# Optimization experiments

Hardware: AMD Instinct MI355X
Metric: run time of the kernel (lower is better)

## Reference

```python
import jax, jax.numpy as jnp
import numpy as np

D_MODEL, D_BLOOM, N_HEADS = 768, 64, 4
HEAD_DIM = D_MODEL // N_HEADS


def setup_inputs() -> dict:
    key = jax.random.key(0)
    ks = jax.random.split(key, 16)
    B, S = 8, 1024
    s = 0.02
    return {
        "dnabert_hidden": jax.random.normal(ks[0], (B, S, D_MODEL), jnp.float32),
        "bloom_encoding": jax.random.uniform(ks[1], (B, S, D_BLOOM), jnp.float32),
        "Wq": jax.random.normal(ks[2], (D_MODEL, D_MODEL), jnp.float32) * s,
        "bq": jnp.zeros((D_MODEL,), jnp.float32),
        "Wk": jax.random.normal(ks[3], (D_BLOOM, D_MODEL), jnp.float32) * s,
        "bk": jnp.zeros((D_MODEL,), jnp.float32),
        "Wv": jax.random.normal(ks[4], (D_MODEL, D_MODEL), jnp.float32) * s,
        "bv": jnp.zeros((D_MODEL,), jnp.float32),
        "Wb1": jax.random.normal(ks[5], (D_BLOOM, N_HEADS * 2), jnp.float32) * s,
        "bb1": jnp.zeros((N_HEADS * 2,), jnp.float32),
        "Wb2": jax.random.normal(ks[6], (N_HEADS * 2, N_HEADS), jnp.float32) * s,
        "bb2": jnp.zeros((N_HEADS,), jnp.float32),
        "Wo": jax.random.normal(ks[7], (D_MODEL, D_MODEL), jnp.float32) * s,
        "bo": jnp.zeros((D_MODEL,), jnp.float32),
        "ln_g": jnp.ones((D_MODEL,), jnp.float32),
        "ln_b": jnp.zeros((D_MODEL,), jnp.float32),
    }


def reference(dnabert_hidden, bloom_encoding, Wq, bq, Wk, bk, Wv, bv,
              Wb1, bb1, Wb2, bb2, Wo, bo, ln_g, ln_b):
    B, S, _ = dnabert_hidden.shape
    H, Dh = N_HEADS, HEAD_DIM
    # projections -> [B, H, S, Dh]
    Q = (dnabert_hidden @ Wq + bq).reshape(B, S, H, Dh).transpose(0, 2, 1, 3)
    K = (bloom_encoding @ Wk + bk).reshape(B, S, H, Dh).transpose(0, 2, 1, 3)
    V = (dnabert_hidden @ Wv + bv).reshape(B, S, H, Dh).transpose(0, 2, 1, 3)
    scores = jnp.einsum('bhqd,bhkd->bhqk', Q, K) / jnp.sqrt(jnp.float32(Dh))
    # bloom bias MLP: [B, S, H] -> broadcast over query positions as [B, H, 1, S]
    h = jax.nn.gelu(bloom_encoding @ Wb1 + bb1, approximate=False)
    bias = (h @ Wb2 + bb2).transpose(0, 2, 1)[:, :, None, :]
    attn = jax.nn.softmax(scores + bias, axis=-1)  # dropout is identity in eval
    ctx = jnp.einsum('bhqk,bhkd->bhqd', attn, V)
    ctx = ctx.transpose(0, 2, 1, 3).reshape(B, S, H * Dh)
    out = ctx @ Wo + bo
    x = out + dnabert_hidden
    mu = jnp.mean(x, axis=-1, keepdims=True)
    var = jnp.var(x, axis=-1, keepdims=True)
    y = (x - mu) * jax.lax.rsqrt(var + 1e-5) * ln_g + ln_b
    return y, attn
```

## Files before the change

### kernel.cpp

```cpp
#include <hip/hip_runtime.h>
#include <hip/hip_bf16.h>
#include <math.h>
#include <stdint.h>

typedef __bf16 bf16;
typedef __bf16 bf16x8 __attribute__((ext_vector_type(8)));
typedef __bf16 bf16x4v __attribute__((ext_vector_type(4)));
typedef float f32x4 __attribute__((ext_vector_type(4)));

#define NHEADS 4
#define DM 768
#define DB 64
#define HD 192
#define BATCH 8
#define SEQ 1024
#define MROWS 8192
#define SCALE 0.07216878364870323f

__device__ __forceinline__ void gld_lds16(const void* g, void* l) {
  __builtin_amdgcn_global_load_lds(
      (__attribute__((address_space(1))) void*)(void*)g,
      (__attribute__((address_space(3))) void*)l, 16, 0, 0);
}

__global__ __launch_bounds__(256) void prologue(
    const float* __restrict__ Xd, bf16* __restrict__ Xd_bf,
    const float* __restrict__ Xb, bf16* __restrict__ Xb_bf,
    const float* __restrict__ Wq, const float* __restrict__ Wv,
    const float* __restrict__ Wk, const float* __restrict__ Wo,
    bf16* __restrict__ WT0, bf16* __restrict__ WT1,
    bf16* __restrict__ WT2, bf16* __restrict__ WT3,
    const float* __restrict__ Wb1, const float* __restrict__ bb1,
    const float* __restrict__ Wb2, const float* __restrict__ bb2,
    float* __restrict__ biasarr) {
  const int id = blockIdx.x;
  const int tid = threadIdx.x;
  if (id < 6656) {
    const float* in = (id < 6144) ? Xd : Xb;
    bf16* out = (id < 6144) ? Xd_bf : Xb_bf;
    long i = (long)(id < 6144 ? id : id - 6144) * 256 + tid;
    f32x4 v = *(const f32x4*)&in[i * 4];
    bf16x4v t;
    t[0] = (bf16)v[0]; t[1] = (bf16)v[1]; t[2] = (bf16)v[2]; t[3] = (bf16)v[3];
    *(bf16x4v*)&out[i * 4] = t;
  } else if (id < 6688) {
    int idx = (id - 6656) * 256 + tid;
    const float* x = Xb + (long)idx * DB;
    float h[8];
#pragma unroll
    for (int j = 0; j < 8; ++j) h[j] = bb1[j];
    for (int k = 0; k < DB; ++k) {
      float xv = x[k];
#pragma unroll
      for (int j = 0; j < 8; ++j) h[j] = fmaf(xv, Wb1[k * 8 + j], h[j]);
    }
#pragma unroll
    for (int j = 0; j < 8; ++j) {
      float a = h[j];
      h[j] = 0.5f * a * (1.0f + erff(a * 0.7071067811865476f));
    }
    int b = idx >> 10, s = idx & 1023;
#pragma unroll
    for (int o = 0; o < 4; ++o) {
      float a = bb2[o];
#pragma unroll
      for (int j = 0; j < 8; ++j) a = fmaf(h[j], Wb2[j * 4 + o], a);
      biasarr[((long)(b * 4 + o) << 10) + s] = a;
    }
  } else {
    int wi = id - 6688;
    const float* W;
    bf16* WT;
    int K, base;
    if (wi < 2304)      { W = Wq; WT = WT0; K = DM; base = 0; }
    else if (wi < 4608) { W = Wv; WT = WT1; K = DM; base = 2304; }
    else if (wi < 4800) { W = Wk; WT = WT2; K = DB; base = 4608; }
    else                { W = Wo; WT = WT3; K = DM; base = 4800; }
    long idx = (long)(wi - base) * 256 + tid;
    if (idx >= (long)K * DM) return;
    int k = (int)(idx % K);
    int n = (int)(idx / K);
    WT[(long)n * K + k] = (bf16)W[(long)k * DM + n];
  }
}

__global__ __launch_bounds__(256) void rowsum_scale_f32(float* __restrict__ attn) {
  const int row = blockIdx.x * 4 + (threadIdx.x >> 6);
  const int lane = threadIdx.x & 63;
  float* ar = attn + ((long)row << 10);
  f32x4 v[4];
#pragma unroll
  for (int i = 0; i < 4; ++i) v[i] = *(const f32x4*)&ar[i * 256 + lane * 4];
  float s = 0.0f;
#pragma unroll
  for (int i = 0; i < 4; ++i)
#pragma unroll
    for (int j = 0; j < 4; ++j) s += v[i][j];
  for (int d = 1; d < 64; d <<= 1) s += __shfl_xor(s, d);
  float iv = 1.0f / s;
#pragma unroll
  for (int i = 0; i < 4; ++i) {
#pragma unroll
    for (int j = 0; j < 4; ++j) v[i][j] *= iv;
    *(f32x4*)&ar[i * 256 + lane * 4] = v[i];
  }
}

template <int MODE>
__global__ __launch_bounds__(256) void gemm_bt(
    const bf16* __restrict__ A, int lda,
    const bf16* __restrict__ BT, int ldb,
    const float* __restrict__ Af,
    int M, int N, int Kd,
    const float* __restrict__ cb1,
    const float* __restrict__ cb2,
    const float* __restrict__ resid,
    void* __restrict__ out, void* __restrict__ out2) {
  __shared__ __attribute__((aligned(16))) bf16 aL[2 * 128 * 32];
  __shared__ __attribute__((aligned(16))) bf16 bL[2 * 128 * 32];
  __shared__ float ivL[128];
  const int tid = threadIdx.x;
  const int lane = tid & 63;
  const int wid = tid >> 6;
  const int wr = wid >> 1, wc = wid & 1;
  int bx, by, bz;
  if constexpr (MODE == 2 || MODE == 7) {
    int idd = blockIdx.x;
    bz = idd & 31;
    int t = idd >> 5;
    bx = t & 7;
    by = t >> 3;
  } else if constexpr (MODE == 5 || MODE == 8) {
    int idd = blockIdx.x;
    bz = idd & 31;
    bx = (idd >> 5) & 1;
    by = idd >> 6;
  } else {
    bx = blockIdx.x; by = blockIdx.y; bz = 0;
  }
  const int m0 = by * 128, n0 = bx * 128;

  const bf16* Ab = A;
  const bf16* Bb = BT;
  const float* Afb = Af;
  if constexpr (MODE == 2 || MODE == 7) {
    long o = ((long)((bz >> 2) * SEQ)) * DM + (long)(bz & 3) * HD;
    Ab = A + o;
    Bb = BT + o;
  }
  if constexpr (MODE == 8) {
    Ab = A + ((long)bz << 20);
    Bb = BT + (((long)((bz >> 2) * DM + (bz & 3) * HD)) << 10);
  }
  if constexpr (MODE == 5) {
    Bb = BT + (((long)((bz >> 2) * DM + (bz & 3) * HD)) << 10);
    Afb = Af + ((long)bz << 20);
  }

  float iv0 = 0.f, iv1 = 0.f;
  if constexpr (MODE == 8) {
    if (tid < 128) {
      const float* p = cb2 + ((((long)bz << 10) + m0 + tid) << 4);
      float s = 0.0f;
#pragma unroll
      for (int i = 0; i < 16; ++i) s += p[i];
      ivL[tid] = 1.0f / s;
    }
    __syncthreads();
    iv0 = ivL[tid >> 2];
    iv1 = ivL[64 + (tid >> 2)];
  }

  f32x4 acc[4][4] = {};

  for (int k0 = 0; k0 < Kd; k0 += 64) {
#pragma unroll
    for (int h = 0; h < 2; ++h) {
      if constexpr (MODE == 5) {
#pragma unroll
        for (int p = 0; p < 2; ++p) {
          int f = (p * 256 + tid) * 8;
          int row = f >> 5, col = f & 31;
          const float* g = Afb + (long)(m0 + row) * lda + k0 + h * 32 + col;
          f32x4 x0 = *(const f32x4*)g;
          f32x4 x1 = *(const f32x4*)(g + 4);
          bf16x8 t;
          t[0] = (bf16)x0[0]; t[1] = (bf16)x0[1]; t[2] = (bf16)x0[2]; t[3] = (bf16)x0[3];
          t[4] = (bf16)x1[0]; t[5] = (bf16)x1[1]; t[6] = (bf16)x1[2]; t[7] = (bf16)x1[3];
          *(bf16x8*)&aL[h * 4096 + f] = t;
        }
      } else {
#pragma unroll
        for (int p = 0; p < 2; ++p) {
          int f = (p * 256 + tid) * 8;
          int row = f >> 5, col = f & 31;
          gld_lds16(Ab + (long)(m0 + row) * lda + k0 + h * 32 + col, &aL[h * 4096 + f]);
        }
      }
#pragma unroll
      for (int p = 0; p < 2; ++p) {
        int f = (p * 256 + tid) * 8;
        int row = f >> 5, col = f & 31;
        int nn = n0 + row;
        nn = nn < N ? nn : N - 1;
        gld_lds16(Bb + (long)nn * ldb + k0 + h * 32 + col, &bL[h * 4096 + f]);
      }
    }
    __syncthreads();

    if constexpr (MODE == 8) {
      if ((k0 < 512) == (bx == 0)) {
#pragma unroll
        for (int h = 0; h < 2; ++h)
#pragma unroll
          for (int p = 0; p < 2; ++p) {
            int f = (p * 256 + tid) * 8;
            int row = f >> 5, col = f & 31;
            bf16x8 e = *(const bf16x8*)&aL[h * 4096 + f];
            float iv = p ? iv1 : iv0;
            f32x4 w0, w1;
            w0[0] = (float)e[0] * iv; w0[1] = (float)e[1] * iv;
            w0[2] = (float)e[2] * iv; w0[3] = (float)e[3] * iv;
            w1[0] = (float)e[4] * iv; w1[1] = (float)e[5] * iv;
            w1[2] = (float)e[6] * iv; w1[3] = (float)e[7] * iv;
            float* ap = (float*)out2 + ((long)bz << 20) + ((long)(m0 + row) << 10)
                        + k0 + h * 32 + col;
            __builtin_nontemporal_store(w0, (f32x4*)ap);
            __builtin_nontemporal_store(w1, (f32x4*)(ap + 4));
          }
      }
    }

    const int rsel = lane & 15, ksel = (lane >> 4) * 8;
#pragma unroll
    for (int h = 0; h < 2; ++h) {
      bf16x8 af[4], bfr[4];
#pragma unroll
      for (int m = 0; m < 4; ++m)
        af[m] = *(const bf16x8*)&aL[h * 4096 + (wr * 64 + m * 16 + rsel) * 32 + ksel];
#pragma unroll
      for (int n = 0; n < 4; ++n)
        bfr[n] = *(const bf16x8*)&bL[h * 4096 + (wc * 64 + n * 16 + rsel) * 32 + ksel];
#pragma unroll
      for (int m = 0; m < 4; ++m)
#pragma unroll
        for (int n = 0; n < 4; ++n)
          acc[m][n] = __builtin_amdgcn_mfma_f32_16x16x32_bf16(af[m], bfr[n], acc[m][n], 0, 0, 0);
    }
    __syncthreads();
  }

  const int rl = (lane >> 4) * 4, cl = lane & 15;

  if constexpr (MODE == 2) {
    float bvv[4];
#pragma unroll
    for (int n = 0; n < 4; ++n)
      bvv[n] = cb2[(bz << 10) + n0 + wc * 64 + n * 16 + cl];
#pragma unroll
    for (int m = 0; m < 4; ++m)
#pragma unroll
      for (int n = 0; n < 4; ++n)
#pragma unroll
        for (int j = 0; j < 4; ++j)
          acc[m][n][j] = __expf(fmaf(acc[m][n][j], SCALE, bvv[n]));
    float* part = (float*)out2;
#pragma unroll
    for (int m = 0; m < 4; ++m) {
#pragma unroll
      for (int j = 0; j < 4; ++j) {
        float s = acc[m][0][j] + acc[m][1][j] + acc[m][2][j] + acc[m][3][j];
#pragma unroll
        for (int d = 1; d < 16; d <<= 1) s += __shfl_xor(s, d);
        if (cl == 0) {
          int mg = m0 + wr * 64 + m * 16 + rl + j;
          part[((((long)bz << 10) + mg) << 4) + bx * 2 + wc] = s;
        }
      }
    }
#pragma unroll
    for (int m = 0; m < 4; ++m)
#pragma unroll
      for (int n = 0; n < 4; ++n)
#pragma unroll
        for (int j = 0; j < 4; ++j) {
          int row = wr * 64 + m * 16 + rl + j;
          int col = wc * 64 + n * 16 + cl;
          bf16* Lt = (row < 64) ? &aL[row * 128 + col] : &bL[(row - 64) * 128 + col];
          *Lt = (bf16)acc[m][n][j];
        }
    __syncthreads();
#pragma unroll
    for (int it = 0; it < 8; ++it) {
      int row = it * 16 + (tid >> 4);
      int col = (tid & 15) * 8;
      bf16x8 v = (row < 64) ? *(const bf16x8*)&aL[row * 128 + col]
                            : *(const bf16x8*)&bL[(row - 64) * 128 + col];
      *(bf16x8*)&((bf16*)out)[((long)bz << 20) + ((long)(m0 + row) << 10) + n0 + col] = v;
    }
    return;
  }

  if constexpr (MODE == 6) {
    if (n0 >= DM) {
      const int d0 = n0 - DM;
      float bvv[4];
#pragma unroll
      for (int n = 0; n < 4; ++n)
        bvv[n] = cb2[d0 + wc * 64 + n * 16 + cl];
#pragma unroll
      for (int m = 0; m < 4; ++m)
#pragma unroll
        for (int n = 0; n < 4; ++n)
#pragma unroll
          for (int j = 0; j < 4; ++j) {
            int row = wr * 64 + m * 16 + rl + j;
            int col = wc * 64 + n * 16 + cl;
            int sw = row ^ ((col & 7) << 4);
            bf16 val = (bf16)(acc[m][n][j] + bvv[n]);
            if (col < 64) aL[col * 128 + sw] = val;
            else          bL[(col - 64) * 128 + sw] = val;
          }
      __syncthreads();
      const int b = m0 >> 10, s0 = m0 & 1023;
#pragma unroll
      for (int it = 0; it < 8; ++it) {
        int d = it * 16 + (tid >> 4);
        int s = (tid & 15) * 8;
        int sw = s ^ ((d & 7) << 4);
        bf16x8 v = (d < 64) ? *(const bf16x8*)&aL[d * 128 + sw]
                            : *(const bf16x8*)&bL[(d - 64) * 128 + sw];
        *(bf16x8*)&((bf16*)out2)[((long)(b * DM + d0 + d) << 10) + s0 + s] = v;
      }
      return;
    }
  }

#pragma unroll
  for (int m = 0; m < 4; ++m) {
#pragma unroll
    for (int n = 0; n < 4; ++n) {
      int ng = n0 + wc * 64 + n * 16 + cl;
      if (ng >= N) continue;
#pragma unroll
      for (int j = 0; j < 4; ++j) {
        int mg = m0 + wr * 64 + m * 16 + rl + j;
        float v = acc[m][n][j];
        if constexpr (MODE == 0) {
          ((bf16*)out)[(long)mg * DM + ng] = (bf16)(v + cb1[ng]);
        } else if constexpr (MODE == 7) {
          ((float*)out)[((long)bz << 20) + ((long)mg << 10) + ng] =
              __expf(fmaf(v, SCALE, cb2[(bz << 10) + ng]));
        } else if constexpr (MODE == 8) {
          ((bf16*)out)[(long)((bz >> 2) * SEQ + mg) * DM + (bz & 3) * HD + ng] =
              (bf16)(v * ivL[wr * 64 + m * 16 + rl + j]);
        } else if constexpr (MODE == 5) {
          ((bf16*)out)[(long)((bz >> 2) * SEQ + mg) * DM + (bz & 3) * HD + ng] = (bf16)v;
        } else if constexpr (MODE == 6) {
          ((bf16*)out)[(long)mg * DM + ng] = (bf16)(v + cb1[ng]);
        } else {
          long o = (long)mg * DM + ng;
          ((float*)out)[o] = v + cb1[ng] + resid[o];
        }
      }
    }
  }
}

__global__ __launch_bounds__(256) void layernorm_rows(float* x, const float* __restrict__ gam,
                                                      const float* __restrict__ bet) {
  int row = blockIdx.x * 4 + (threadIdx.x >> 6);
  int lane = threadIdx.x & 63;
  float* r = x + (long)row * DM;
  f32x4 v[3];
#pragma unroll
  for (int i = 0; i < 3; ++i) v[i] = *(const f32x4*)&r[i * 256 + lane * 4];
  float s = 0.0f, ss = 0.0f;
#pragma unroll
  for (int i = 0; i < 3; ++i)
#pragma unroll
    for (int j = 0; j < 4; ++j) {
      s += v[i][j];
      ss += v[i][j] * v[i][j];
    }
  for (int d = 1; d < 64; d <<= 1) {
    s += __shfl_xor(s, d);
    ss += __shfl_xor(ss, d);
  }
  float mu = s * (1.0f / 768.0f);
  float var = ss * (1.0f / 768.0f) - mu * mu;
  float rs = 1.0f / sqrtf(var + 1e-5f);
#pragma unroll
  for (int i = 0; i < 3; ++i) {
#pragma unroll
    for (int j = 0; j < 4; ++j) {
      int c = i * 256 + lane * 4 + j;
      v[i][j] = (v[i][j] - mu) * rs * gam[c] + bet[c];
    }
    *(f32x4*)&r[i * 256 + lane * 4] = v[i];
  }
}

extern "C" void kernel_launch(void* const* d_in, const int* in_sizes, int n_in,
                              void* d_out, int out_size, void* d_ws, size_t ws_size,
                              hipStream_t stream) {
  const float* Xd = (const float*)d_in[0];
  const float* Xb = (const float*)d_in[1];
  const float* Wq = (const float*)d_in[2];
  const float* bq = (const float*)d_in[3];
  const float* Wk = (const float*)d_in[4];
  const float* bk = (const float*)d_in[5];
  const float* Wv = (const float*)d_in[6];
  const float* bv = (const float*)d_in[7];
  const float* Wb1 = (const float*)d_in[8];
  const float* bb1 = (const float*)d_in[9];
  const float* Wb2 = (const float*)d_in[10];
  const float* bb2 = (const float*)d_in[11];
  const float* Wo = (const float*)d_in[12];
  const float* bo = (const float*)d_in[13];
  const float* lng = (const float*)d_in[14];
  const float* lnb = (const float*)d_in[15];

  float* y = (float*)d_out;
  float* attn = y + (long)MROWS * DM;

  char* w = (char*)d_ws;
  bf16* Xd_bf = (bf16*)w; w += (long)MROWS * DM * 2;
  bf16* Xb_bf = (bf16*)w; w += (long)MROWS * DB * 2;
  bf16* WqvT = (bf16*)w; w += (long)2 * DM * DM * 2;
  bf16* WkT = (bf16*)w; w += (long)DM * DB * 2;
  bf16* WoT = (bf16*)w; w += (long)DM * DM * 2;
  bf16* Qb = (bf16*)w; w += (long)MROWS * DM * 2;
  bf16* Kb = (bf16*)w; w += (long)MROWS * DM * 2;
  bf16* VTb = (bf16*)w; w += (long)MROWS * DM * 2;
  float* biasarr = (float*)w; w += (long)BATCH * NHEADS * SEQ * 4;
  float* part = (float*)w; w += (long)32 * SEQ * 16 * 4;
  bf16* Sb = (bf16*)w; w += (long)32 * SEQ * SEQ * 2;
  const bool useS = ((size_t)(w - (char*)d_ws)) <= ws_size;
  bf16* ctxb = Xd_bf;

  dim3 blk(256);
  prologue<<<13792, blk, 0, stream>>>(Xd, Xd_bf, Xb, Xb_bf, Wq, Wv, Wk, Wo,
                                      WqvT, WqvT + (long)DM * DM, WkT, WoT,
                                      Wb1, bb1, Wb2, bb2, biasarr);

  gemm_bt<0><<<dim3(6, 64, 1), blk, 0, stream>>>(Xb_bf, DB, WkT, DB, nullptr, MROWS, DM, DB,
                                                 bk, nullptr, nullptr, Kb, nullptr);
  gemm_bt<6><<<dim3(12, 64, 1), blk, 0, stream>>>(Xd_bf, DM, WqvT, DM, nullptr, MROWS, 2 * DM, DM,
                                                  bq, bv, nullptr, Qb, VTb);
  if (useS) {
    gemm_bt<2><<<2048, blk, 0, stream>>>(Qb, DM, Kb, DM, nullptr, SEQ, SEQ, HD,
                                         nullptr, biasarr, nullptr, Sb, part);
    gemm_bt<8><<<512, blk, 0, stream>>>(Sb, SEQ, VTb, SEQ, nullptr, SEQ, HD, SEQ,
                                        nullptr, part, nullptr, ctxb, attn);
  } else {
    gemm_bt<7><<<2048, blk, 0, stream>>>(Qb, DM, Kb, DM, nullptr, SEQ, SEQ, HD,
                                         nullptr, biasarr, nullptr, attn, nullptr);
    rowsum_scale_f32<<<8192, blk, 0, stream>>>(attn);
    gemm_bt<5><<<512, blk, 0, stream>>>(nullptr, SEQ, VTb, SEQ, attn, SEQ, HD, SEQ,
                                        nullptr, nullptr, nullptr, ctxb, nullptr);
  }
  gemm_bt<4><<<dim3(6, 64, 1), blk, 0, stream>>>(ctxb, DM, WoT, DM, nullptr, MROWS, DM, DM,
                                                 bo, nullptr, Xd, y, nullptr);
  layernorm_rows<<<2048, 256, 0, stream>>>(y, lng, lnb);
}
```

Measured before the change: 193.5 us.

## Tile weight transpose through LDS and stage GEMM epilogues for vector stores

Replaces the per-element strided weight transpose in the prologue with 64x64 tiles staged in padded shared memory, so reads and writes are both coalesced and bf16 outputs are written eight at a time. Also stages the bf16 outputs of the projection GEMMs (modes 0/6) and the attention-context GEMM (mode 8) through LDS, replacing scattered 2-byte stores with 16-byte row-contiguous stores. This removes uncoalesced global writes at the cost of an extra LDS round trip and barrier in each epilogue. The prologue grid shrinks to match the tiled layout, and the prologue now declares shared memory for every block, including the conversion blocks that do not use it.

```diff
diff --git a/kernel.cpp b/kernel.cpp
--- a/kernel.cpp
+++ b/kernel.cpp
@@ -33,6 +33,7 @@
     const float* __restrict__ Wb1, const float* __restrict__ bb1,
     const float* __restrict__ Wb2, const float* __restrict__ bb2,
     float* __restrict__ biasarr) {
+  __shared__ float Lt[64 * 65];
   const int id = blockIdx.x;
   const int tid = threadIdx.x;
   if (id < 6656) {
@@ -71,16 +72,31 @@
     int wi = id - 6688;
     const float* W;
     bf16* WT;
-    int K, base;
-    if (wi < 2304)      { W = Wq; WT = WT0; K = DM; base = 0; }
-    else if (wi < 4608) { W = Wv; WT = WT1; K = DM; base = 2304; }
-    else if (wi < 4800) { W = Wk; WT = WT2; K = DB; base = 4608; }
-    else                { W = Wo; WT = WT3; K = DM; base = 4800; }
-    long idx = (long)(wi - base) * 256 + tid;
-    if (idx >= (long)K * DM) return;
-    int k = (int)(idx % K);
-    int n = (int)(idx / K);
-    WT[(long)n * K + k] = (bf16)W[(long)k * DM + n];
+    int K, tIdx;
+    if (wi < 144)      { W = Wq; WT = WT0; K = DM; tIdx = wi; }
+    else if (wi < 288) { W = Wv; WT = WT1; K = DM; tIdx = wi - 144; }
+    else if (wi < 300) { W = Wk; WT = WT2; K = DB; tIdx = wi - 288; }
+    else               { W = Wo; WT = WT3; K = DM; tIdx = wi - 300; }
+    const int tk0 = (tIdx / 12) * 64;
+    const int tn0 = (tIdx % 12) * 64;
+#pragma unroll
+    for (int p = 0; p < 4; ++p) {
+      int r = p * 16 + (tid >> 4);
+      int c = (tid & 15) * 4;
+      f32x4 v = *(const f32x4*)&W[(long)(tk0 + r) * DM + tn0 + c];
+      Lt[r * 65 + c] = v[0]; Lt[r * 65 + c + 1] = v[1];
+      Lt[r * 65 + c + 2] = v[2]; Lt[r * 65 + c + 3] = v[3];
+    }
+    __syncthreads();
+    const int n = tid >> 2, kg = (tid & 3) * 16;
+    bf16x8 o0, o1;
+#pragma unroll
+    for (int e = 0; e < 8; ++e) {
+      o0[e] = (bf16)Lt[(kg + e) * 65 + n];
+      o1[e] = (bf16)Lt[(kg + 8 + e) * 65 + n];
+    }
+    *(bf16x8*)&WT[(long)(tn0 + n) * K + tk0 + kg] = o0;
+    *(bf16x8*)&WT[(long)(tn0 + n) * K + tk0 + kg + 8] = o1;
   }
 }
 
@@ -336,6 +352,64 @@
     }
   }
 
+  if constexpr (MODE == 0 || MODE == 6) {
+    float bvv[4];
+#pragma unroll
+    for (int n = 0; n < 4; ++n)
+      bvv[n] = cb1[n0 + wc * 64 + n * 16 + cl];
+#pragma unroll
+    for (int m = 0; m < 4; ++m)
+#pragma unroll
+      for (int n = 0; n < 4; ++n)
+#pragma unroll
+        for (int j = 0; j < 4; ++j) {
+          int row = wr * 64 + m * 16 + rl + j;
+          int col = wc * 64 + n * 16 + cl;
+          bf16 val = (bf16)(acc[m][n][j] + bvv[n]);
+          if (row < 64) aL[row * 128 + col] = val;
+          else          bL[(row - 64) * 128 + col] = val;
+        }
+    __syncthreads();
+#pragma unroll
+    for (int it = 0; it < 8; ++it) {
+      int row = it * 16 + (tid >> 4);
+      int col = (tid & 15) * 8;
+      bf16x8 v = (row < 64) ? *(const bf16x8*)&aL[row * 128 + col]
+                            : *(const bf16x8*)&bL[(row - 64) * 128 + col];
+      *(bf16x8*)&((bf16*)out)[(long)(m0 + row) * DM + n0 + col] = v;
+    }
+    return;
+  }
+
+  if constexpr (MODE == 8) {
+#pragma unroll
+    for (int m = 0; m < 4; ++m)
+#pragma unroll
+      for (int n = 0; n < 4; ++n)
+#pragma unroll
+        for (int j = 0; j < 4; ++j) {
+          int row = wr * 64 + m * 16 + rl + j;
+          int col = wc * 64 + n * 16 + cl;
+          bf16 val = (bf16)(acc[m][n][j] * ivL[row]);
+          if (row < 64) aL[row * 128 + col] = val;
+          else          bL[(row - 64) * 128 + col] = val;
+        }
+    __syncthreads();
+    const int b = bz >> 2, h = bz & 3;
+#pragma unroll
+    for (int it = 0; it < 8; ++it) {
+      int row = it * 16 + (tid >> 4);
+      int col = (tid & 15) * 8;
+      int ng = n0 + col;
+      if (ng < HD) {
+        bf16x8 v = (row < 64) ? *(const bf16x8*)&aL[row * 128 + col]
+                              : *(const bf16x8*)&bL[(row - 64) * 128 + col];
+        *(bf16x8*)&((bf16*)out)[(long)(b * SEQ + m0 + row) * DM + h * HD + ng] = v;
+      }
+    }
+    return;
+  }
+
 #pragma unroll
   for (int m = 0; m < 4; ++m) {
 #pragma unroll
@@ -346,18 +420,11 @@
       for (int j = 0; j < 4; ++j) {
         int mg = m0 + wr * 64 + m * 16 + rl + j;
         float v = acc[m][n][j];
-        if constexpr (MODE == 0) {
-          ((bf16*)out)[(long)mg * DM + ng] = (bf16)(v + cb1[ng]);
-        } else if constexpr (MODE == 7) {
+        if constexpr (MODE == 7) {
           ((float*)out)[((long)bz << 20) + ((long)mg << 10) + ng] =
               __expf(fmaf(v, SCALE, cb2[(bz << 10) + ng]));
-        } else if constexpr (MODE == 8) {
-          ((bf16*)out)[(long)((bz >> 2) * SEQ + mg) * DM + (bz & 3) * HD + ng] =
-              (bf16)(v * ivL[wr * 64 + m * 16 + rl + j]);
         } else if constexpr (MODE == 5) {
           ((bf16*)out)[(long)((bz >> 2) * SEQ + mg) * DM + (bz & 3) * HD + ng] = (bf16)v;
-        } else if constexpr (MODE == 6) {
-          ((bf16*)out)[(long)mg * DM + ng] = (bf16)(v + cb1[ng]);
         } else {
           long o = (long)mg * DM + ng;
           ((float*)out)[o] = v + cb1[ng] + resid[o];
@@ -440,9 +507,9 @@
   bf16* ctxb = Xd_bf;
 
   dim3 blk(256);
-  prologue<<<13792, blk, 0, stream>>>(Xd, Xd_bf, Xb, Xb_bf, Wq, Wv, Wk, Wo,
-                                      WqvT, WqvT + (long)DM * DM, WkT, WoT,
-                                      Wb1, bb1, Wb2, bb2, biasarr);
+  prologue<<<7132, blk, 0, stream>>>(Xd, Xd_bf, Xb, Xb_bf, Wq, Wv, Wk, Wo,
+                                     WqvT, WqvT + (long)DM * DM, WkT, WoT,
+                                     Wb1, bb1, Wb2, bb2, biasarr);
 
   gemm_bt<0><<<dim3(6, 64, 1), blk, 0, stream>>>(Xb_bf, DB, WkT, DB, nullptr, MROWS, DM, DB,
                                                  bk, nullptr, nullptr, Kb, nullptr);
```

Result: faster. 187.2 us (-3.3%).
